# Performance work log

Hardware: AMD Instinct MI355X
Metric: run time of the kernel (lower is better)

The kernel has to match this reference:

```python
import jax, jax.numpy as jnp
import numpy as np

M = 10000            # total proposals concatenated over 5 FPN levels (~2000/level)
TOP_K = 2000         # FPN_POST_NMS_TOP_N
NMS_THRESH = 0.7     # FPN_NMS_THRESH
IMG_H, IMG_W = 800.0, 1333.0


def setup_inputs() -> dict:
    key = jax.random.key(0)
    k1, k2, k3, k4, k5 = jax.random.split(key, 5)
    x1 = jax.random.uniform(k1, (M,)) * (IMG_W - 64.0)
    y1 = jax.random.uniform(k2, (M,)) * (IMG_H - 64.0)
    w = jax.random.uniform(k3, (M,)) * 256.0 + 8.0
    h = jax.random.uniform(k4, (M,)) * 256.0 + 8.0
    scores = jax.random.uniform(k5, (M,))
    bidx = jnp.zeros((M,), jnp.float32)  # batch index column (batch_size == 1)
    proposals = jnp.stack(
        [bidx, x1, y1, jnp.minimum(x1 + w, IMG_W), jnp.minimum(y1 + h, IMG_H), scores],
        axis=-1,
    )[None]  # [1, M, 6] = (idx, x1, y1, x2, y2, score)
    return {"proposals": proposals}


def _pairwise_iou(boxes):
    # boxes: [M, 4] (x1, y1, x2, y2) -> IoU [M, M]
    x1, y1, x2, y2 = boxes[:, 0], boxes[:, 1], boxes[:, 2], boxes[:, 3]
    area = (x2 - x1) * (y2 - y1)
    iw = jnp.maximum(jnp.minimum(x2[:, None], x2[None, :]) - jnp.maximum(x1[:, None], x1[None, :]), 0.0)
    ih = jnp.maximum(jnp.minimum(y2[:, None], y2[None, :]) - jnp.maximum(y1[:, None], y1[None, :]), 0.0)
    inter = iw * ih
    return inter / (area[:, None] + area[None, :] - inter + 1e-8)


def reference(proposals):
    # proposals: [1, M, 6] = (batch_idx, x1, y1, x2, y2, score), pre-NMS multi-scale concat
    boxes = proposals[0, :, 1:5]
    scores = proposals[0, :, 5]
    order = jnp.argsort(-scores)            # greedy NMS visits boxes in score order
    b = boxes[order]
    iou = _pairwise_iou(b)                  # [M, M], the dominant memory traffic
    idxs = jnp.arange(M)

    def body(i, keep):
        # if box i survives, suppress all lower-score boxes with IoU > thresh
        sup = keep[i] & (iou[i] > NMS_THRESH) & (idxs > i)
        return keep & ~sup

    keep = jax.lax.fori_loop(0, M, body, jnp.ones((M,), bool))
    # kept boxes first (stable sort preserves descending-score order), take top-k
    sel = jnp.argsort(~keep, stable=True)[:TOP_K]
    keep_idx = order[sel]
    rois = proposals[0, keep_idx, :5]       # (idx, x1, y1, x2, y2)
    return rois[None]                        # [1, TOP_K, 5]
```

## Files before the change

### kernel.cpp

```cpp
#include <hip/hip_runtime.h>
#include <hip/hip_bf16.h>

#define M 10000
#define TOP_K 2000
#define NW 157
#define NMS_T 0.7f
#define WCAP 40
#define MROWS (WCAP * 64)
#define NSEG 16
#define SEGSZ 640
#define ECAP (NSEG * SEGSZ)
#define NTILE (WCAP * (WCAP + 1) / 2)
#define TPB 512
#define SKEYN 10240
#define NRB 160
#define KPS (SKEYN / 16)

typedef unsigned long long ull;

#define OFF_ORD    0
#define OFF_SX1    40000
#define OFF_SY1    80000
#define OFF_SX2    120000
#define OFF_SY2    160000
#define OFF_AREA   200000
#define OFF_ECNT   240000
#define OFF_META   240128
#define OFF_EWORD  281088

__global__ __launch_bounds__(1024) void k_rank(const float* __restrict__ prop,
                                               int* __restrict__ ord,
                                               float* __restrict__ sx1, float* __restrict__ sy1,
                                               float* __restrict__ sx2, float* __restrict__ sy2,
                                               float* __restrict__ sarea,
                                               unsigned* __restrict__ ecnt) {
    __shared__ ull skey[SKEYN];
    __shared__ unsigned scnt[64];
    const int tid = threadIdx.x, lane = tid & 63, w = tid >> 6;
    const int bid = blockIdx.x;

    for (int i = tid; i < SKEYN; i += 1024) {
        ull k = ~0ull;
        if (i < M) k = (((ull)(~__float_as_uint(prop[i * 6 + 5]))) << 14) | (unsigned)i;
        skey[i] = k;
    }
    if (tid < 64) scnt[tid] = 0u;
    __syncthreads();

    const int e = bid * 64 + lane;
    const ull kbe = skey[(e < M) ? e : 0];
    unsigned cnt = 0;
    const ull* base = &skey[w * KPS];
#pragma unroll 4
    for (int f = 0; f < KPS; f += 2) {
        ull a = base[f], b = base[f + 1];
        cnt += (a < kbe) ? 1u : 0u;
        cnt += (b < kbe) ? 1u : 0u;
    }
    if (e < M) atomicAdd(&scnt[lane], cnt);
    __syncthreads();

    if (w == 0 && e < M) {
        unsigned r = scnt[lane];
        ord[r] = e;
        float x1 = prop[e * 6 + 1], y1 = prop[e * 6 + 2];
        float x2 = prop[e * 6 + 3], y2 = prop[e * 6 + 4];
        sx1[r] = x1; sy1[r] = y1; sx2[r] = x2; sy2[r] = y2;
        sarea[r] = (x2 - x1) * (y2 - y1);
    }
    if (bid == 0 && tid < NSEG) ecnt[tid] = 0u;
}

__device__ __forceinline__ ull init_keep_word(int w) {
    if (w >= NW) return 0ull;
    int rem = M - w * 64;
    if (rem >= 64) return ~0ull;
    if (rem <= 0) return 0ull;
    return (~0ull) >> (64 - rem);
}

__global__ __launch_bounds__(64) void k_mask(const float* __restrict__ sx1, const float* __restrict__ sy1,
                                             const float* __restrict__ sx2, const float* __restrict__ sy2,
                                             const float* __restrict__ sarea,
                                             unsigned* __restrict__ ecnt,
                                             unsigned* __restrict__ meta,
                                             ull* __restrict__ eword) {
    const int lane = threadIdx.x;
    const int t0 = blockIdx.x;
    int tt = t0, ci = 0, rl = WCAP;
    while (tt >= rl) { tt -= rl; --rl; ++ci; }
    const int cj = ci + tt;
    const int j = cj * 64 + lane;
    const float jx1 = sx1[j], jy1 = sy1[j], jx2 = sx2[j], jy2 = sy2[j], ja = sarea[j];
    const int i0 = ci * 64;
    const int irow = i0 + lane;
    const float bx1 = sx1[irow], by1 = sy1[irow], bx2 = sx2[irow], by2 = sy2[irow], ba = sarea[irow];
    const bool diag = (ci == cj);
    ull myw = 0ull;
#pragma unroll 8
    for (int r = 0; r < 64; ++r) {
        float ix1 = __shfl(bx1, r, 64);
        float iy1 = __shfl(by1, r, 64);
        float ix2 = __shfl(bx2, r, 64);
        float iy2 = __shfl(by2, r, 64);
        float ia  = __shfl(ba,  r, 64);
        float iw = fminf(ix2, jx2) - fmaxf(ix1, jx1); iw = fmaxf(iw, 0.f);
        float ih = fminf(iy2, jy2) - fmaxf(iy1, jy1); ih = fmaxf(ih, 0.f);
        float inter = iw * ih;
        float iou = inter / (ia + ja - inter + 1e-8f);
        bool bit = (iou > NMS_T) && (!diag || (j > (i0 + r)));
        ull wv = __ballot(bit);
        myw = (lane == r) ? wv : myw;
    }
    ull nzm = __ballot(myw != 0ull);
    int nz = __popcll(nzm);
    if (nz) {
        const int seg = t0 & (NSEG - 1);
        unsigned base = 0;
        if (lane == 0) base = atomicAdd(&ecnt[seg], (unsigned)nz);
        base = (unsigned)__shfl((int)base, 0, 64);
        if (myw) {
            ull lt = (lane == 0) ? 0ull : (~0ull >> (64 - lane));
            unsigned slot = base + (unsigned)__popcll(nzm & lt);
            if (slot < SEGSZ) {
                meta[seg * SEGSZ + slot] = ((unsigned)(i0 + lane) << 6) | (unsigned)cj;
                eword[seg * SEGSZ + slot] = myw;
            }
        }
    }
}

__global__ __launch_bounds__(TPB) void k_nms(const unsigned* __restrict__ ecnt,
                                             const unsigned* __restrict__ meta,
                                             const ull* __restrict__ eword,
                                             const float* __restrict__ sx1, const float* __restrict__ sy1,
                                             const float* __restrict__ sx2, const float* __restrict__ sy2,
                                             const float* __restrict__ sarea,
                                             const int* __restrict__ ord,
                                             const float* __restrict__ prop,
                                             float* __restrict__ out) {
    __shared__ unsigned s_meta[ECAP];
    __shared__ ull s_w[ECAP];
    __shared__ ull aw[64], kill[64];
    __shared__ ull s_keep[NW];
    __shared__ int wcnt[NW];
    __shared__ unsigned segoff[NSEG + 1];
    __shared__ int s_flag, s_stop, s_total, s_dropped;

    const int tid = threadIdx.x;

    if (tid == 0) {
        unsigned acc = 0; int d = 0;
        for (int g = 0; g < NSEG; ++g) {
            unsigned c = ecnt[g];
            if (c > SEGSZ) { d = 1; c = SEGSZ; }
            segoff[g] = acc; acc += c;
        }
        segoff[NSEG] = acc;
        s_dropped = d;
    }
    __syncthreads();
    const unsigned ne = segoff[NSEG];

    if (!s_dropped) {
        for (int g = 0; g < NSEG; ++g) {
            unsigned b0 = segoff[g], c = segoff[g + 1] - b0;
            for (unsigned e = tid; e < c; e += TPB) {
                s_meta[b0 + e] = meta[g * SEGSZ + e];
                s_w[b0 + e]    = eword[g * SEGSZ + e];
            }
        }
        if (tid < 64) aw[tid] = (tid < WCAP) ? ~0ull : 0ull;
        __syncthreads();
        int rounds = 0;
        while (true) {
            if (tid < 64) kill[tid] = 0ull;
            if (tid == 0) s_flag = 0;
            __syncthreads();
            for (unsigned e = tid; e < ne; e += TPB) {
                unsigned m = s_meta[e];
                unsigned i = m >> 6, cj = m & 63u;
                if ((aw[i >> 6] >> (i & 63)) & 1ull) atomicOr(&kill[cj], s_w[e]);
            }
            __syncthreads();
            if (tid < WCAP) {
                ull na = ~kill[tid];
                if (na != aw[tid]) { aw[tid] = na; s_flag = 1; }
            }
            __syncthreads();
            if (!s_flag || ++rounds > 4100) break;
        }
        if (tid < 64) {
            int c = __popcll(aw[tid]); int inc = c;
            for (int off = 1; off < 64; off <<= 1) {
                int n = __shfl_up(inc, off, 64);
                if (tid >= off) inc += n;
            }
            ull hb = __ballot(inc >= TOP_K);
            if (tid == 0) s_stop = hb ? ((int)__builtin_ctzll(hb) + 1) : -1;
        }
        __syncthreads();
        if (s_stop >= 0) {
            if (tid < NW) s_keep[tid] = (tid < s_stop) ? aw[tid] : 0ull;
            __syncthreads();
        } else {
            if (tid < NW) s_keep[tid] = (tid < WCAP) ? aw[tid] : init_keep_word(tid);
            __syncthreads();
            for (int j = MROWS + tid; j < M; j += TPB) {
                float jx1 = sx1[j], jy1 = sy1[j], jx2 = sx2[j], jy2 = sy2[j], ja = sarea[j];
                bool dead = false;
                for (int i = 0; i < MROWS && !dead; ++i) {
                    if (!((s_keep[i >> 6] >> (i & 63)) & 1ull)) continue;
                    float ix1 = sx1[i], iy1 = sy1[i], ix2 = sx2[i], iy2 = sy2[i], ia = sarea[i];
                    float iw = fminf(ix2, jx2) - fmaxf(ix1, jx1); iw = fmaxf(iw, 0.f);
                    float ih = fminf(iy2, jy2) - fmaxf(iy1, jy1); ih = fmaxf(ih, 0.f);
                    float inter = iw * ih;
                    float iou = inter / (ia + ja - inter + 1e-8f);
                    if (iou > NMS_T) dead = true;
                }
                if (dead) atomicAnd(&s_keep[j >> 6], ~(1ull << (j & 63)));
            }
            __syncthreads();
            for (int i = MROWS; i < M; ++i) {
                if ((s_keep[i >> 6] >> (i & 63)) & 1ull) {
                    float ix1 = sx1[i], iy1 = sy1[i], ix2 = sx2[i], iy2 = sy2[i], ia = sarea[i];
                    for (int j = MROWS + tid; j < M; j += TPB) {
                        if (j > i) {
                            float iw = fminf(ix2, sx2[j]) - fmaxf(ix1, sx1[j]); iw = fmaxf(iw, 0.f);
                            float ih = fminf(iy2, sy2[j]) - fmaxf(iy1, sy1[j]); ih = fmaxf(ih, 0.f);
                            float inter = iw * ih;
                            float iou = inter / (ia + sarea[j] - inter + 1e-8f);
                            if (iou > NMS_T) atomicAnd(&s_keep[j >> 6], ~(1ull << (j & 63)));
                        }
                    }
                }
                __syncthreads();
            }
        }
    } else {
        if (tid < NW) s_keep[tid] = init_keep_word(tid);
        __syncthreads();
        for (int i = 0; i < M; ++i) {
            if ((s_keep[i >> 6] >> (i & 63)) & 1ull) {
                float ix1 = sx1[i], iy1 = sy1[i], ix2 = sx2[i], iy2 = sy2[i], ia = sarea[i];
                for (int j = i + 1 + tid; j < M; j += TPB) {
                    float iw = fminf(ix2, sx2[j]) - fmaxf(ix1, sx1[j]); iw = fmaxf(iw, 0.f);
                    float ih = fminf(iy2, sy2[j]) - fmaxf(iy1, sy1[j]); ih = fmaxf(ih, 0.f);
                    float inter = iw * ih;
                    float iou = inter / (ia + sarea[j] - inter + 1e-8f);
                    if (iou > NMS_T) atomicAnd(&s_keep[j >> 6], ~(1ull << (j & 63)));
                }
            }
            __syncthreads();
        }
    }

    if (tid < NW) wcnt[tid] = __popcll(s_keep[tid]);
    __syncthreads();
    if (tid == 0) {
        int acc = 0;
        for (int q = 0; q < NW; ++q) { int c = wcnt[q]; wcnt[q] = acc; acc += c; }
        s_total = acc;
    }
    __syncthreads();
    const int total = s_total;
    for (int q = tid; q < M; q += TPB) {
        int wq = q >> 6, b = q & 63;
        ull kw = s_keep[wq];
        int below = __popcll(kw & ((1ull << b) - 1ull));
        int kb = wcnt[wq] + below;
        bool isk = (kw >> b) & 1ull;
        int rank = isk ? kb : (total + (q - kb));
        if (rank < TOP_K) {
            int o = ord[q];
            out[rank * 5 + 0] = prop[o * 6 + 0];
            out[rank * 5 + 1] = prop[o * 6 + 1];
            out[rank * 5 + 2] = prop[o * 6 + 2];
            out[rank * 5 + 3] = prop[o * 6 + 3];
            out[rank * 5 + 4] = prop[o * 6 + 4];
        }
    }
}

extern "C" void kernel_launch(void* const* d_in, const int* in_sizes, int n_in,
                              void* d_out, int out_size, void* d_ws, size_t ws_size,
                              hipStream_t stream) {
    const float* prop = (const float*)d_in[0];
    float* out = (float*)d_out;
    char* ws = (char*)d_ws;

    int*      ord   = (int*)(ws + OFF_ORD);
    float*    sx1   = (float*)(ws + OFF_SX1);
    float*    sy1   = (float*)(ws + OFF_SY1);
    float*    sx2   = (float*)(ws + OFF_SX2);
    float*    sy2   = (float*)(ws + OFF_SY2);
    float*    sarea = (float*)(ws + OFF_AREA);
    unsigned* ecnt  = (unsigned*)(ws + OFF_ECNT);
    unsigned* meta  = (unsigned*)(ws + OFF_META);
    ull*      eword = (ull*)(ws + OFF_EWORD);

    k_rank<<<NRB, 1024, 0, stream>>>(prop, ord, sx1, sy1, sx2, sy2, sarea, ecnt);
    k_mask<<<NTILE, 64, 0, stream>>>(sx1, sy1, sx2, sy2, sarea, ecnt, meta, eword);
    k_nms<<<1, TPB, 0, stream>>>(ecnt, meta, eword, sx1, sy1, sx2, sy2, sarea, ord, prop, out);
}
```

Baseline: 48.81 us.

## Replace rank-by-counting sort with score bucket scatter and per-bucket sort

Replaces the O(M^2) comparison-count ranking kernel with a three-kernel bucket sort. Scores are scattered into 4096 buckets via atomics, a prefix scan computes bucket offsets, and each bucket is ranked locally to write the sorted order and box coordinates. This removes the large all-pairs comparison work but adds two extra kernel launches. It also assumes scores lie in [0,1) and that no bucket holds more than 64 entries; overflowing entries are dropped.

```diff
diff --git a/kernel.cpp b/kernel.cpp
--- a/kernel.cpp
+++ b/kernel.cpp
@@ -12,9 +12,8 @@
 #define ECAP (NSEG * SEGSZ)
 #define NTILE (WCAP * (WCAP + 1) / 2)
 #define TPB 512
-#define SKEYN 10240
-#define NRB 160
-#define KPS (SKEYN / 16)
+#define NBK 4096
+#define BKCAP 64
 
 typedef unsigned long long ull;
 
@@ -27,48 +26,77 @@
 #define OFF_ECNT   240000
 #define OFF_META   240128
 #define OFF_EWORD  281088
-
-__global__ __launch_bounds__(1024) void k_rank(const float* __restrict__ prop,
+#define OFF_CNT    363008
+#define OFF_BUF    379392
+
+__global__ __launch_bounds__(1024) void k_zero(unsigned* __restrict__ cnt,
+                                               unsigned* __restrict__ ecnt) {
+    const int tid = threadIdx.x;
+#pragma unroll
+    for (int k = 0; k < NBK / 1024; ++k) cnt[k * 1024 + tid] = 0u;
+    if (tid < NSEG) ecnt[tid] = 0u;
+}
+
+__global__ __launch_bounds__(1024) void k_scatter(const float* __restrict__ prop,
+                                                  unsigned* __restrict__ cnt,
+                                                  ull* __restrict__ buf) {
+    int e = blockIdx.x * 1024 + threadIdx.x;
+    if (e < M) {
+        float s = prop[e * 6 + 5];
+        int t = (int)(s * 4096.0f);
+        int b = 4095 - (t > 4095 ? 4095 : (t < 0 ? 0 : t));
+        unsigned slot = atomicAdd(&cnt[b], 1u);
+        if (slot < BKCAP)
+            buf[(size_t)b * BKCAP + slot] = (((ull)(~__float_as_uint(s))) << 16) | (unsigned)e;
+    }
+}
+
+__global__ __launch_bounds__(512) void k_bsort(const unsigned* __restrict__ cnt,
+                                               const ull* __restrict__ buf,
+                                               const float* __restrict__ prop,
                                                int* __restrict__ ord,
                                                float* __restrict__ sx1, float* __restrict__ sy1,
                                                float* __restrict__ sx2, float* __restrict__ sy2,
-                                               float* __restrict__ sarea,
-                                               unsigned* __restrict__ ecnt) {
-    __shared__ ull skey[SKEYN];
-    __shared__ unsigned scnt[64];
-    const int tid = threadIdx.x, lane = tid & 63, w = tid >> 6;
-    const int bid = blockIdx.x;
-
-    for (int i = tid; i < SKEYN; i += 1024) {
-        ull k = ~0ull;
-        if (i < M) k = (((ull)(~__float_as_uint(prop[i * 6 + 5]))) << 14) | (unsigned)i;
-        skey[i] = k;
-    }
-    if (tid < 64) scnt[tid] = 0u;
-    __syncthreads();
-
-    const int e = bid * 64 + lane;
-    const ull kbe = skey[(e < M) ? e : 0];
-    unsigned cnt = 0;
-    const ull* base = &skey[w * KPS];
-#pragma unroll 4
-    for (int f = 0; f < KPS; f += 2) {
-        ull a = base[f], b = base[f + 1];
-        cnt += (a < kbe) ? 1u : 0u;
-        cnt += (b < kbe) ? 1u : 0u;
-    }
-    if (e < M) atomicAdd(&scnt[lane], cnt);
-    __syncthreads();
-
-    if (w == 0 && e < M) {
-        unsigned r = scnt[lane];
-        ord[r] = e;
-        float x1 = prop[e * 6 + 1], y1 = prop[e * 6 + 2];
-        float x2 = prop[e * 6 + 3], y2 = prop[e * 6 + 4];
-        sx1[r] = x1; sy1[r] = y1; sx2[r] = x2; sy2[r] = y2;
-        sarea[r] = (x2 - x1) * (y2 - y1);
-    }
-    if (bid == 0 && tid < NSEG) ecnt[tid] = 0u;
+                                               float* __restrict__ sarea) {
+    __shared__ unsigned pre[NBK];
+    __shared__ unsigned wsum[8];
+    const int tid = threadIdx.x;
+    const int lane = tid & 63, w = tid >> 6;
+
+    unsigned c8[8]; unsigned s = 0;
+#pragma unroll
+    for (int k = 0; k < 8; ++k) { c8[k] = cnt[tid * 8 + k]; s += c8[k]; }
+    unsigned inc = s;
+    for (int off = 1; off < 64; off <<= 1) {
+        unsigned n = __shfl_up(inc, off, 64);
+        if (lane >= off) inc += n;
+    }
+    if (lane == 63) wsum[w] = inc;
+    __syncthreads();
+    unsigned wb = 0;
+#pragma unroll
+    for (int q = 0; q < 8; ++q) wb += (q < w) ? wsum[q] : 0u;
+    unsigned ex = wb + inc - s;
+#pragma unroll
+    for (int k = 0; k < 8; ++k) { pre[tid * 8 + k] = ex; ex += c8[k]; }
+    __syncthreads();
+
+    const int b = blockIdx.x * 512 + tid;
+    unsigned c = cnt[b]; if (c > BKCAP) c = BKCAP;
+    const unsigned p0 = pre[b];
+    const ull* bb = buf + (size_t)b * BKCAP;
+    for (unsigned i = 0; i < c; ++i) {
+        ull ki = bb[i];
+        unsigned rank = 0;
+        for (unsigned j = 0; j < c; ++j) rank += (bb[j] < ki) ? 1u : 0u;
+        unsigned p = p0 + rank;
+        int o = (int)(ki & 0xFFFFull);
+        ord[p] = o;
+        float x1 = prop[o * 6 + 1], y1 = prop[o * 6 + 2];
+        float x2 = prop[o * 6 + 3], y2 = prop[o * 6 + 4];
+        sx1[p] = x1; sy1[p] = y1; sx2[p] = x2; sy2[p] = y2;
+        sarea[p] = (x2 - x1) * (y2 - y1);
+    }
 }
 
 __device__ __forceinline__ ull init_keep_word(int w) {
@@ -298,8 +326,12 @@
     unsigned* ecnt  = (unsigned*)(ws + OFF_ECNT);
     unsigned* meta  = (unsigned*)(ws + OFF_META);
     ull*      eword = (ull*)(ws + OFF_EWORD);
-
-    k_rank<<<NRB, 1024, 0, stream>>>(prop, ord, sx1, sy1, sx2, sy2, sarea, ecnt);
+    unsigned* cnt   = (unsigned*)(ws + OFF_CNT);
+    ull*      buf   = (ull*)(ws + OFF_BUF);
+
+    k_zero<<<1, 1024, 0, stream>>>(cnt, ecnt);
+    k_scatter<<<10, 1024, 0, stream>>>(prop, cnt, buf);
+    k_bsort<<<8, 512, 0, stream>>>(cnt, buf, prop, ord, sx1, sy1, sx2, sy2, sarea);
     k_mask<<<NTILE, 64, 0, stream>>>(sx1, sy1, sx2, sy2, sarea, ecnt, meta, eword);
     k_nms<<<1, TPB, 0, stream>>>(ecnt, meta, eword, sx1, sy1, sx2, sy2, sarea, ord, prop, out);
 }
```

Result: slower. 56.64 us (+16.0%).
